# Kernel tuning notes

Hardware: AMD Instinct MI355X
Metric: run time of the kernel (lower is better)

## Reference

```python
import jax, jax.numpy as jnp
import numpy as np

N = 65536      # voxels
NFIX = 4096    # fixed-BC voxels (x == 0)
H = 128        # MLP hidden width
NFORCE = 4096  # force-surface points
E0 = 1.0
NU = 0.3
PENAL = 3.0
EM_V = 1e-3    # element volume
L_FIX = 0.05   # BC ramp length for analytical fixed-BC scale
K_FIX = E0 * 100.0
NUM_HUTCH = 50


def mlp(params, x):
    W1, b1, W2, b2, W3, b3, W4, b4 = params
    h = jnp.tanh(x @ W1 + b1)
    h = jnp.tanh(h @ W2 + b2)
    h = jnp.tanh(h @ W3 + b3)
    return h @ W4 + b4


def bc_scale(coord):
    # analytical fixed-BC scale: 0 exactly on the fixed face (x==0), ramps to 1
    return jnp.clip(coord[..., 0] / L_FIX, 0.0, 1.0)


def hutchinson_trace(params, coords, key, num_samples=NUM_HUTCH):
    # tr(J J^T) estimate via v^T J J^T v = ||J^T v||^2, batched VJPs (replaces
    # the per-sample autograd.grad python loop).
    out, vjp_fn = jax.vjp(lambda p: mlp(p, coords), params)

    def step(acc, k):
        v = jax.random.normal(k, out.shape, dtype=out.dtype)
        (g,) = vjp_fn(v)
        flat = jnp.concatenate([x.reshape(-1) for x in jax.tree_util.tree_leaves(g)])
        return acc + flat @ flat, None

    keys = jax.random.split(key, num_samples)
    tot, _ = jax.lax.scan(step, jnp.float32(0.0), keys)
    return tot / num_samples


def setup_inputs() -> dict:
    key = jax.random.key(0)
    ks = jax.random.split(key, 12)
    coord = jax.random.uniform(ks[0], (N, 3), dtype=jnp.float32)
    coord = coord.at[:, 0].set(0.02 + 0.98 * coord[:, 0])  # free voxels: x > 0
    coord = coord.at[:NFIX, 0].set(0.0)                    # fixed voxels: x == 0
    xPhys_m = jax.random.uniform(ks[1], (N, 1), dtype=jnp.float32)
    def lin(k, fi, fo):
        return jax.random.normal(k, (fi, fo), dtype=jnp.float32) / jnp.sqrt(jnp.float32(fi))
    W1 = lin(ks[2], 3, H); b1 = jnp.zeros((H,), jnp.float32)
    W2 = lin(ks[3], H, H); b2 = jnp.zeros((H,), jnp.float32)
    W3 = lin(ks[4], H, H); b3 = jnp.zeros((H,), jnp.float32)
    W4 = lin(ks[5], H, 3); b4 = jnp.zeros((3,), jnp.float32)
    force_coords = jax.random.uniform(ks[6], (NFORCE, 3), dtype=jnp.float32)
    F_vector = jax.random.normal(ks[7], (3,), dtype=jnp.float32)
    return dict(xPhys_m=xPhys_m, coord=coord, W1=W1, b1=b1, W2=W2, b2=b2,
                W3=W3, b3=b3, W4=W4, b4=b4, force_coords=force_coords,
                F_vector=F_vector, n_fix=NFIX)


def reference(xPhys_m, coord, W1, b1, W2, b2, W3, b3, W4, b4,
              force_coords, F_vector, n_fix):
    params = (W1, b1, W2, b2, W3, b3, W4, b4)

    u = mlp(params, coord)                       # [N,3] displacements
    scale = bc_scale(coord)                      # [N]
    fixed_mask = (scale == 0.0)

    # fixed-BC penalty energy
    u_fix = u * fixed_mask[:, None].astype(u.dtype)
    E_fix_all = xPhys_m ** PENAL * 0.5 * K_FIX * jnp.sum(u_fix ** 2, axis=1, keepdims=True)
    n_fix_ratio = jnp.float32(n_fix) / jnp.float32(N)
    E_fix = jnp.mean(E_fix_all[:n_fix]) * n_fix_ratio * EM_V

    # NTK-based adaptive weight via Hutchinson trace (detached, like .item())
    hkey = jax.random.key(42)
    ku, kr = jax.random.split(hkey)
    tr_uu = hutchinson_trace(params, coord[:n_fix], ku)
    tr_rr = hutchinson_trace(params, coord[n_fix:], kr)
    lam_fix = jax.lax.stop_gradient(jnp.clip(tr_rr / (tr_uu + 1e-12), 1e-3, 1e3))

    # per-voxel displacement Jacobian J[n, i, j] = d u_i / d coord_j  (batched
    # fwd-mode replaces three autograd.grad calls)
    J = jax.vmap(jax.jacfwd(lambda c: mlp(params, c)))(coord)  # [N,3,3]
    ux = J[:, 1, :]   # grads of u[:,1] (u0 in source)
    uy = J[:, 0, :]   # grads of u[:,0] (u1 in source)
    uz = J[:, 2, :]
    eps11 = ux[:, 1]
    eps12 = 0.5 * ux[:, 0] + 0.5 * uy[:, 1]
    eps13 = 0.5 * ux[:, 2] + 0.5 * uz[:, 1]
    eps22 = uy[:, 0]
    eps23 = 0.5 * uy[:, 2] + 0.5 * uz[:, 0]
    eps33 = uz[:, 2]

    lame_mu = E0 / (2.0 * (1.0 + NU))
    lame_lambda = E0 * NU / ((1.0 + NU) * (1.0 - 2.0 * NU))
    tr_strain = eps11 + eps22 + eps33
    sq_diag = eps11 * eps11 + eps22 * eps22 + eps33 * eps33
    energy = (0.5 * lame_lambda * tr_strain * tr_strain
              + lame_mu * (sq_diag + 2.0 * (eps12 * eps12 + eps13 * eps13 + eps23 * eps23)))
    energy = energy[:, None] * xPhys_m ** PENAL   # [N,1]
    energy_c = energy * 2.0
    energy_ans = EM_V * jnp.mean(energy)

    force_l = jnp.sum(mlp(params, force_coords) @ F_vector)

    loss = energy_ans - force_l + lam_fix * E_fix
    return (loss, energy_c, u)
```

## Files before the change

### kernel.cpp

```cpp
#include <hip/hip_runtime.h>
#include <math.h>

typedef __bf16 bf16x8 __attribute__((ext_vector_type(8)));
typedef __bf16 bf16x4 __attribute__((ext_vector_type(4)));
typedef float f32x4 __attribute__((ext_vector_type(4)));

#define HDIM 128
#define NTHREADS 512

#define EMV 0.001f
#define LFIX 0.05f
#define KFIX 100.0f
#define LAMBDA_L 0.5769230769230769f
#define MU_L 0.3846153846153846f

__device__ __forceinline__ int swb(int r, int blk) {
    return (r << 7) + ((blk ^ (r & 7)) << 3);
}
__device__ __forceinline__ int swb32(int r, int g) {
    return (r << 5) + ((g ^ ((r >> 1) & 3)) << 3);
}

__device__ __forceinline__ float fast_tanh(float x) {
    float e = __expf(2.f * x);
    return 1.f - 2.f * __builtin_amdgcn_rcpf(e + 1.f);
}

__device__ __forceinline__ float wred(float v) {
#pragma unroll
    for (int off = 32; off > 0; off >>= 1) v += __shfl_down(v, off, 64);
    return v;
}

template <int NB, int CT0, int CT1>
__device__ __forceinline__ void gemm_f8(const bf16x8 (&aw)[4],
                                        __bf16* const* inb, __bf16* const* outb,
                                        const float* __restrict__ bsL,
                                        int wid, int l15, int q) {
    f32x4 acc[NB][CT1 - CT0];
#pragma unroll
    for (int b = 0; b < NB; ++b)
#pragma unroll
        for (int c = 0; c < CT1 - CT0; ++c) acc[b][c] = (f32x4){0.f, 0.f, 0.f, 0.f};

#pragma unroll
    for (int s = 0; s < 4; ++s)
#pragma unroll
        for (int b = 0; b < NB; ++b)
#pragma unroll
            for (int c = CT0; c < CT1; ++c) {
                bf16x8 bfr = *(const bf16x8*)(inb[b] + swb(c * 16 + l15, s * 4 + q));
                acc[b][c - CT0] = __builtin_amdgcn_mfma_f32_16x16x32_bf16(
                    aw[s], bfr, acc[b][c - CT0], 0, 0, 0);
            }
    __syncthreads();
    const int n0 = wid * 16 + q * 4;
    float4 bv = *(const float4*)(bsL + n0);
    float bias4[4] = {bv.x, bv.y, bv.z, bv.w};
#pragma unroll
    for (int c = CT0; c < CT1; ++c) {
        const int p = c * 16 + l15;
        const int widx = swb(p, n0 >> 3) + (n0 & 7);
        bf16x4 hv;
        float fct[4];
#pragma unroll
        for (int i = 0; i < 4; ++i) {
            float h = fast_tanh(acc[0][c - CT0][i] + bias4[i]);
            hv[i] = (__bf16)h;
            fct[i] = 1.f - h * h;
        }
        *(bf16x4*)(outb[0] + widx) = hv;
#pragma unroll
        for (int b = 1; b < NB; ++b) {
            bf16x4 ov;
#pragma unroll
            for (int i = 0; i < 4; ++i) ov[i] = (__bf16)(acc[b][c - CT0][i] * fct[i]);
            *(bf16x4*)(outb[b] + widx) = ov;
        }
    }
}

template <int NB>
__device__ __forceinline__ void gemm_tr8(const float* __restrict__ Wg, __bf16* Wst,
                                         __bf16* const* bufs,
                                         const __bf16* __restrict__ href,
                                         int wid, int l15, int q, int tid) {
    f32x4 acc[NB][2];
#pragma unroll
    for (int b = 0; b < NB; ++b) {
        acc[b][0] = (f32x4){0.f, 0.f, 0.f, 0.f};
        acc[b][1] = (f32x4){0.f, 0.f, 0.f, 0.f};
    }
#pragma unroll
    for (int c = 0; c < 4; ++c) {
        __syncthreads();
        {
            int j = tid >> 2, k8 = tid & 3;
            const float4* src = (const float4*)(Wg + j * HDIM + c * 32 + k8 * 8);
            float4 v0 = src[0], v1 = src[1];
            bf16x8 pk = {(__bf16)v0.x, (__bf16)v0.y, (__bf16)v0.z, (__bf16)v0.w,
                         (__bf16)v1.x, (__bf16)v1.y, (__bf16)v1.z, (__bf16)v1.w};
            *(bf16x8*)(Wst + swb32(j, k8)) = pk;
        }
        __syncthreads();
        bf16x8 afr = *(const bf16x8*)(Wst + swb32(wid * 16 + l15, q));
#pragma unroll
        for (int b = 0; b < NB; ++b) {
            bf16x8 b0 = *(const bf16x8*)(bufs[b] + swb(l15, c * 4 + q));
            acc[b][0] = __builtin_amdgcn_mfma_f32_16x16x32_bf16(afr, b0, acc[b][0], 0, 0, 0);
            bf16x8 b1 = *(const bf16x8*)(bufs[b] + swb(16 + l15, c * 4 + q));
            acc[b][1] = __builtin_amdgcn_mfma_f32_16x16x32_bf16(afr, b1, acc[b][1], 0, 0, 0);
        }
    }
    __syncthreads();
    const int n0 = wid * 16 + q * 4;
#pragma unroll
    for (int ct = 0; ct < 2; ++ct) {
        const int p = ct * 16 + l15;
        const int widx = swb(p, n0 >> 3) + (n0 & 7);
        bf16x4 hv = *(const bf16x4*)(href + widx);
        float fct[4];
#pragma unroll
        for (int i = 0; i < 4; ++i) {
            float h = (float)hv[i];
            fct[i] = 1.f - h * h;
        }
#pragma unroll
        for (int b = 0; b < NB; ++b) {
            bf16x4 ov;
#pragma unroll
            for (int i = 0; i < 4; ++i) ov[i] = (__bf16)(acc[b][ct][i] * fct[i]);
            *(bf16x4*)(bufs[b] + widx) = ov;
        }
    }
}

__device__ __forceinline__ void dnorms8(const __bf16* a, const __bf16* b, const __bf16* c2,
                                        float* npart, int tid) {
    int p = tid & 31, cc = tid >> 5;
    bf16x8 v0 = *(const bf16x8*)(a + swb(p, cc));
    bf16x8 v1 = *(const bf16x8*)(b + swb(p, cc));
    bf16x8 v2 = *(const bf16x8*)(c2 + swb(p, cc));
    float s0 = 0.f, s1 = 0.f, s2 = 0.f;
#pragma unroll
    for (int e = 0; e < 8; ++e) {
        float f0 = (float)v0[e], f1 = (float)v1[e], f2 = (float)v2[e];
        s0 += f0 * f0;
        s1 += f1 * f1;
        s2 += f2 * f2;
    }
    npart[(0 + cc) * 32 + p] = s0;
    npart[(16 + cc) * 32 + p] = s1;
    npart[(32 + cc) * 32 + p] = s2;
}

__device__ __forceinline__ float sum16(const float* npart, int buf, int p) {
    float d = 0.f;
#pragma unroll
    for (int i = 0; i < 16; ++i) d += npart[(buf * 16 + i) * 32 + p];
    return d;
}
__device__ __forceinline__ float sum48(const float* npart, int p) {
    float d = 0.f;
#pragma unroll
    for (int i = 0; i < 48; ++i) d += npart[i * 32 + p];
    return d;
}

__global__ void __launch_bounds__(NTHREADS, 4) pinn_all(
    const float* __restrict__ xPhys, const float* __restrict__ coord,
    const float* __restrict__ W1, const float* __restrict__ b1,
    const float* __restrict__ W2, const float* __restrict__ b2,
    const float* __restrict__ W3, const float* __restrict__ b3,
    const float* __restrict__ W4, const float* __restrict__ b4,
    const float* __restrict__ fc, const float* __restrict__ Fv,
    const int* __restrict__ nfixp,
    float* __restrict__ energy_c_out, float* __restrict__ u_out,
    float* __restrict__ acc, int nm32, int nmain64, int ntrb, int NF) {
    __shared__ __align__(16) __bf16 pool[32768];
    __shared__ __align__(16) __bf16 W4p[16 * HDIM];
    __shared__ __align__(16) float W1s[4 * HDIM];
    __shared__ __align__(16) float W4ts[3 * HDIM];
    __shared__ __align__(16) float gls[64 * 12];
    __shared__ __align__(16) float uls[64 * 4];
    __shared__ float nh1s[32], nh2s[32], nh3s[32];

    const int tid = threadIdx.x;
    const int lane = tid & 63, wid = tid >> 6, l15 = lane & 15, q = lane >> 4;
    const int bi = blockIdx.x;
    const int nfixv = nfixp[0];

    int ttile = -1;
    if (bi < ntrb) {
        const int nfull = nfixv >> 5;
        const int cm = (nfixv & 31) ? 1 : 0;
        const int c1 = (nfull + 7) >> 3;
        int t;
        if (bi < c1) {
            t = bi << 3;
        } else if (cm && bi == c1) {
            t = nfull;
        } else {
            const int rr0 = nfull + cm;
            const int f0 = rr0 + ((8 - (rr0 & 15) + 16) & 15);
            t = f0 + ((bi - c1 - cm) << 4);
        }
        if (t >= nm32) return;
        ttile = t;
    }

    float px0, px1, px2;
    if (bi < ntrb) {
        const float* cp = coord + (ttile * 32 + (lane & 31)) * 3;
        px0 = cp[0]; px1 = cp[1]; px2 = cp[2];
    } else if (bi < ntrb + nmain64) {
        const float* cp = coord + ((bi - ntrb) * 64 + lane) * 3;
        px0 = cp[0]; px1 = cp[1]; px2 = cp[2];
    } else {
        int pp = (bi - ntrb - nmain64) * 64 + lane;
        if (pp >= NF) pp = NF - 1;
        const float* cp = fc + pp * 3;
        px0 = cp[0]; px1 = cp[1]; px2 = cp[2];
    }

    for (int i = tid; i < 3 * HDIM; i += NTHREADS) W1s[i] = W1[i];
    if (tid < HDIM) W1s[3 * HDIM + tid] = b1[tid];
    if (tid < 3 * HDIM) W4ts[tid] = W4[(tid & 127) * 3 + (tid >> 7)];
    if (tid < 256) {
        int o = tid >> 4, blk = tid & 15, j0 = blk * 8;
        bf16x8 pk;
#pragma unroll
        for (int e = 0; e < 8; ++e) pk[e] = (__bf16)((o < 3) ? W4[(j0 + e) * 3 + o] : 0.f);
        *(bf16x8*)(W4p + swb(o, blk)) = pk;
    }
    bf16x8 aw2[4], aw3[4];
#pragma unroll
    for (int s = 0; s < 4; ++s) {
        const int kb = s * 32 + q * 8;
        const int n = wid * 16 + l15;
        bf16x8 v2, v3;
#pragma unroll
        for (int e = 0; e < 8; ++e) {
            v2[e] = (__bf16)W2[(kb + e) * HDIM + n];
            v3[e] = (__bf16)W3[(kb + e) * HDIM + n];
        }
        aw2[s] = v2;
        aw3[s] = v3;
    }
    __syncthreads();

    if (bi < ntrb) {
        const int base = ttile * 32;
        __bf16* H1 = pool;
        __bf16* H2 = pool + 4096;
        __bf16* H3 = pool + 8192;
        __bf16* T0 = pool + 12288;
        __bf16* T1 = pool + 16384;
        __bf16* T2 = pool + 20480;
        __bf16* WST = pool + 24576;
        float* npart = (float*)(pool + 28672);

        {
            const int p = lane & 31, sub = lane >> 5;
            const int blk = wid * 2 + sub, j0 = blk * 8;
            bf16x8 hv, t0v, t1v, t2v;
#pragma unroll
            for (int jj = 0; jj < 8; ++jj) {
                int j = j0 + jj;
                float w0 = W1s[j], w1 = W1s[HDIM + j], w2 = W1s[2 * HDIM + j];
                float z = W1s[3 * HDIM + j] + px0 * w0 + px1 * w1 + px2 * w2;
                float h = fast_tanh(z);
                float fct = 1.f - h * h;
                hv[jj] = (__bf16)h;
                t0v[jj] = (__bf16)(fct * w0);
                t1v[jj] = (__bf16)(fct * w1);
                t2v[jj] = (__bf16)(fct * w2);
            }
            int wi = swb(p, blk);
            *(bf16x8*)(H1 + wi) = hv;
            *(bf16x8*)(T0 + wi) = t0v;
            *(bf16x8*)(T1 + wi) = t1v;
            *(bf16x8*)(T2 + wi) = t2v;
        }
        __syncthreads();
        {
            __bf16* ib[4] = {H1, T0, T1, T2};
            __bf16* ob[4] = {H2, T0, T1, T2};
            gemm_f8<4, 0, 2>(aw2, ib, ob, b2, wid, l15, q);
        }
        __syncthreads();
        {
            __bf16* ib[4] = {H2, T0, T1, T2};
            __bf16* ob[4] = {H3, T0, T1, T2};
            gemm_f8<4, 0, 2>(aw3, ib, ob, b3, wid, l15, q);
        }
        __syncthreads();

        dnorms8(H1, H2, H3, npart, tid);
        __syncthreads();
        if (tid < 32) {
            nh1s[tid] = sum16(npart, 0, tid);
            nh2s[tid] = sum16(npart, 1, tid);
            nh3s[tid] = sum16(npart, 2, tid);
        }
        __syncthreads();
        {
            const int p = lane & 31, sub = lane >> 5;
            const int blk = wid * 2 + sub, j0 = blk * 8;
            bf16x8 h3v = *(const bf16x8*)(H3 + swb(p, blk));
            bf16x8 d0, d1, d2;
#pragma unroll
            for (int e = 0; e < 8; ++e) {
                float h = (float)h3v[e];
                float fct = 1.f - h * h;
                d0[e] = (__bf16)(fct * W4ts[j0 + e]);
                d1[e] = (__bf16)(fct * W4ts[HDIM + j0 + e]);
                d2[e] = (__bf16)(fct * W4ts[2 * HDIM + j0 + e]);
            }
            int wi = swb(p, blk);
            *(bf16x8*)(T0 + wi) = d0;
            *(bf16x8*)(T1 + wi) = d1;
            *(bf16x8*)(T2 + wi) = d2;
        }
        __syncthreads();
        float s_acc = 0.f;
        dnorms8(T0, T1, T2, npart, tid);
        __syncthreads();
        if (tid < 32) s_acc = sum48(npart, tid) * (1.f + nh2s[tid]);
        {
            __bf16* ib[3] = {T0, T1, T2};
            gemm_tr8<3>(W3, WST, ib, H2, wid, l15, q, tid);
        }
        __syncthreads();
        dnorms8(T0, T1, T2, npart, tid);
        __syncthreads();
        if (tid < 32) s_acc += sum48(npart, tid) * (1.f + nh1s[tid]);
        {
            __bf16* ib[3] = {T0, T1, T2};
            gemm_tr8<3>(W2, WST, ib, H1, wid, l15, q, tid);
        }
        __syncthreads();
        dnorms8(T0, T1, T2, npart, tid);
        __syncthreads();
        if (tid < 64) {
            float su = 0.f, sr = 0.f, cu = 0.f, cr = 0.f;
            if (tid < 32) {
                int p = tid;
                float nx = px0 * px0 + px1 * px1 + px2 * px2;
                float s = s_acc + sum48(npart, p) * (1.f + nx) + 3.f * (nh3s[p] + 1.f);
                bool uu = (base + p) < nfixv;
                su = uu ? s : 0.f;
                sr = uu ? 0.f : s;
                cu = uu ? 1.f : 0.f;
                cr = uu ? 0.f : 1.f;
            }
            su = wred(su);
            sr = wred(sr);
            cu = wred(cu);
            cr = wred(cr);
            if (tid == 0) {
                atomicAdd(acc + 3, su);
                atomicAdd(acc + 4, sr);
                atomicAdd(acc + 5, cu);
                atomicAdd(acc + 6, cr);
            }
        }
    } else if (bi < ntrb + nmain64) {
        const int base = (bi - ntrb) * 64;
        __bf16* HF = pool;
        __bf16* TF0 = pool + 8192;
        __bf16* TF1 = pool + 16384;
        __bf16* TF2 = pool + 24576;

        {
            const int p = lane;
#pragma unroll
            for (int it2 = 0; it2 < 2; ++it2) {
                const int blk = it2 * 8 + wid, j0 = blk * 8;
                bf16x8 hv, t0v, t1v, t2v;
#pragma unroll
                for (int jj = 0; jj < 8; ++jj) {
                    int j = j0 + jj;
                    float w0 = W1s[j], w1 = W1s[HDIM + j], w2 = W1s[2 * HDIM + j];
                    float z = W1s[3 * HDIM + j] + px0 * w0 + px1 * w1 + px2 * w2;
                    float h = fast_tanh(z);
                    float fct = 1.f - h * h;
                    hv[jj] = (__bf16)h;
                    t0v[jj] = (__bf16)(fct * w0);
                    t1v[jj] = (__bf16)(fct * w1);
                    t2v[jj] = (__bf16)(fct * w2);
                }
                int wi = swb(p, blk);
                *(bf16x8*)(HF + wi) = hv;
                *(bf16x8*)(TF0 + wi) = t0v;
                *(bf16x8*)(TF1 + wi) = t1v;
                *(bf16x8*)(TF2 + wi) = t2v;
            }
        }
        __syncthreads();
        {
            __bf16* ib[4] = {HF, TF0, TF1, TF2};
            gemm_f8<4, 0, 2>(aw2, ib, ib, b2, wid, l15, q);
            gemm_f8<4, 2, 4>(aw2, ib, ib, b2, wid, l15, q);
        }
        __syncthreads();
        {
            __bf16* ib[4] = {HF, TF0, TF1, TF2};
            gemm_f8<4, 0, 2>(aw3, ib, ib, b3, wid, l15, q);
            gemm_f8<4, 2, 4>(aw3, ib, ib, b3, wid, l15, q);
        }
        __syncthreads();

        {
            f32x4 ha0 = (f32x4){0.f, 0.f, 0.f, 0.f};
            f32x4 ha1 = (f32x4){0.f, 0.f, 0.f, 0.f};
            if (wid < 4) {
                const int ct = wid;
#pragma unroll
                for (int s = 0; s < 4; ++s) {
                    int kb = s * 4 + q;
                    bf16x8 af = *(const bf16x8*)(W4p + swb(l15, kb));
                    bf16x8 bA = *(const bf16x8*)(HF + swb(ct * 16 + l15, kb));
                    ha0 = __builtin_amdgcn_mfma_f32_16x16x32_bf16(af, bA, ha0, 0, 0, 0);
                    bf16x8 bB = *(const bf16x8*)(TF0 + swb(ct * 16 + l15, kb));
                    ha1 = __builtin_amdgcn_mfma_f32_16x16x32_bf16(af, bB, ha1, 0, 0, 0);
                }
                if (q == 0) {
                    int p = ct * 16 + l15;
#pragma unroll
                    for (int o = 0; o < 3; ++o) {
                        float uv = ha0[o] + b4[o];
                        uls[p * 4 + o] = uv;
                        u_out[(base + p) * 3 + o] = uv;
                    }
#pragma unroll
                    for (int o = 0; o < 3; ++o) gls[p * 12 + o] = ha1[o];
                }
            } else {
                const int ct = wid - 4;
#pragma unroll
                for (int s = 0; s < 4; ++s) {
                    int kb = s * 4 + q;
                    bf16x8 af = *(const bf16x8*)(W4p + swb(l15, kb));
                    bf16x8 bA = *(const bf16x8*)(TF1 + swb(ct * 16 + l15, kb));
                    ha0 = __builtin_amdgcn_mfma_f32_16x16x32_bf16(af, bA, ha0, 0, 0, 0);
                    bf16x8 bB = *(const bf16x8*)(TF2 + swb(ct * 16 + l15, kb));
                    ha1 = __builtin_amdgcn_mfma_f32_16x16x32_bf16(af, bB, ha1, 0, 0, 0);
                }
                if (q == 0) {
                    int p = ct * 16 + l15;
#pragma unroll
                    for (int o = 0; o < 3; ++o) gls[p * 12 + 3 + o] = ha0[o];
#pragma unroll
                    for (int o = 0; o < 3; ++o) gls[p * 12 + 6 + o] = ha1[o];
                }
            }
        }
        __syncthreads();

        if (tid < 64) {
            int p = tid;
            float xp = xPhys[base + p];
            float xp3 = xp * xp * xp;
            float sc = fminf(fmaxf(px0 * (1.f / LFIX), 0.f), 1.f);
            float ef = 0.f;
            if ((base + p) < nfixv && sc == 0.f) {
                float u0 = uls[p * 4], u1 = uls[p * 4 + 1], u2 = uls[p * 4 + 2];
                ef = xp3 * 0.5f * KFIX * (u0 * u0 + u1 * u1 + u2 * u2);
            }
            float g00 = gls[p * 12 + 0], g01 = gls[p * 12 + 1], g02 = gls[p * 12 + 2];
            float g10 = gls[p * 12 + 3], g11 = gls[p * 12 + 4], g12 = gls[p * 12 + 5];
            float g20 = gls[p * 12 + 6], g21 = gls[p * 12 + 7], g22 = gls[p * 12 + 8];
            float e11 = g11, e22 = g00, e33 = g22;
            float e12 = 0.5f * (g01 + g10);
            float e13 = 0.5f * (g21 + g12);
            float e23 = 0.5f * (g20 + g02);
            float tr = e11 + e22 + e33;
            float en = 0.5f * LAMBDA_L * tr * tr +
                       MU_L * (e11 * e11 + e22 * e22 + e33 * e33 +
                               2.f * (e12 * e12 + e13 * e13 + e23 * e23));
            float exp3 = en * xp3;
            energy_c_out[base + p] = 2.f * exp3;
            float er = exp3;
            ef = wred(ef);
            er = wred(er);
            if (tid == 0) {
                atomicAdd(acc + 1, ef);
                atomicAdd(acc + 0, er);
            }
        }
    } else {
        const int fbase = (bi - ntrb - nmain64) * 64;
        __bf16* HF = pool;
        {
#pragma unroll
            for (int it2 = 0; it2 < 2; ++it2) {
                const int blk = it2 * 8 + wid, j0 = blk * 8;
                bf16x8 hv;
#pragma unroll
                for (int jj = 0; jj < 8; ++jj) {
                    int j = j0 + jj;
                    float z = W1s[3 * HDIM + j] + px0 * W1s[j] + px1 * W1s[HDIM + j] +
                              px2 * W1s[2 * HDIM + j];
                    hv[jj] = (__bf16)fast_tanh(z);
                }
                *(bf16x8*)(HF + swb(lane, blk)) = hv;
            }
        }
        __syncthreads();
        {
            __bf16* ib[1] = {HF};
            gemm_f8<1, 0, 2>(aw2, ib, ib, b2, wid, l15, q);
            gemm_f8<1, 2, 4>(aw2, ib, ib, b2, wid, l15, q);
        }
        __syncthreads();
        {
            __bf16* ib[1] = {HF};
            gemm_f8<1, 0, 2>(aw3, ib, ib, b3, wid, l15, q);
            gemm_f8<1, 2, 4>(aw3, ib, ib, b3, wid, l15, q);
        }
        __syncthreads();
        if (wid < 4) {
            const int ct = wid;
            f32x4 ha = (f32x4){0.f, 0.f, 0.f, 0.f};
#pragma unroll
            for (int s = 0; s < 4; ++s) {
                int kb = s * 4 + q;
                bf16x8 af = *(const bf16x8*)(W4p + swb(l15, kb));
                bf16x8 bf_ = *(const bf16x8*)(HF + swb(ct * 16 + l15, kb));
                ha = __builtin_amdgcn_mfma_f32_16x16x32_bf16(af, bf_, ha, 0, 0, 0);
            }
            if (q == 0) {
                int p = ct * 16 + l15;
#pragma unroll
                for (int o = 0; o < 3; ++o) uls[p * 4 + o] = ha[o] + b4[o];
            }
        }
        __syncthreads();
        if (tid < 64) {
            float fsum = 0.f;
            if (fbase + tid < NF)
                fsum = uls[tid * 4] * Fv[0] + uls[tid * 4 + 1] * Fv[1] +
                       uls[tid * 4 + 2] * Fv[2];
            fsum = wred(fsum);
            if (tid == 0) atomicAdd(acc + 2, fsum);
        }
    }
}

__global__ void pinn_final(const float* __restrict__ acc, float* __restrict__ out,
                           int Ntot, const int* __restrict__ nfixp) {
    float es = acc[0], ef = acc[1], fl = acc[2];
    float su = acc[3], sr = acc[4], cu = acc[5], cr = acc[6];
    float nfix = (float)nfixp[0];
    float tu = su / fmaxf(cu, 1.f) * nfix;
    float tr = sr / fmaxf(cr, 1.f) * ((float)Ntot - nfix);
    float energy_ans = EMV * (es / (float)Ntot);
    float E_fix = ef * EMV / (float)Ntot;
    float lam = tr / (tu + 1e-12f);
    lam = fminf(fmaxf(lam, 0.001f), 1000.f);
    out[0] = energy_ans - fl + lam * E_fix;
}

extern "C" void kernel_launch(void* const* d_in, const int* in_sizes, int n_in,
                              void* d_out, int out_size, void* d_ws, size_t ws_size,
                              hipStream_t stream) {
    const float* xPhys = (const float*)d_in[0];
    const float* coord = (const float*)d_in[1];
    const float* W1 = (const float*)d_in[2];
    const float* b1 = (const float*)d_in[3];
    const float* W2 = (const float*)d_in[4];
    const float* b2 = (const float*)d_in[5];
    const float* W3 = (const float*)d_in[6];
    const float* b3 = (const float*)d_in[7];
    const float* W4 = (const float*)d_in[8];
    const float* b4 = (const float*)d_in[9];
    const float* fc = (const float*)d_in[10];
    const float* Fv = (const float*)d_in[11];
    const int* nfix = (const int*)d_in[12];

    const int N = in_sizes[0];
    const int NF = in_sizes[10] / 3;
    float* out = (float*)d_out;
    float* acc = (float*)d_ws;

    const int nm32 = N / 32;
    const int nmain64 = N / 64;
    const int ntrb = nm32 / 8 + 2;
    const int nforce64 = (NF + 63) / 64;
    const int nblocks = ntrb + nmain64 + nforce64;
    (void)hipMemsetAsync(acc, 0, 8 * sizeof(float), stream);
    pinn_all<<<dim3(nblocks), dim3(NTHREADS), 0, stream>>>(
        xPhys, coord, W1, b1, W2, b2, W3, b3, W4, b4, fc, Fv, nfix,
        out + 1, out + 1 + N, acc, nm32, nmain64, ntrb, NF);
    pinn_final<<<dim3(1), dim3(1), 0, stream>>>(acc, out, N, nfix);
}
```

Measured before the change: 138.4 us.

## Retile main-path layer GEMMs into 32x32 per-wave blocks with per-buffer passes

Each wave now keeps W2/W3 fragments for two 16-column output tiles (a 32-wide column block) and computes a 2x2 tile block over 32 points, so every B fragment loaded from LDS feeds two MFMAs. The main 64-point path processes the hidden activations and the three tangent buffers in separate passes, keeping the tanh derivative factors in registers instead of one combined multi-buffer GEMM split into two halves. This is meant to cut LDS read traffic per MFMA. In exchange it adds more barriers (one per pass) and doubles the weight-fragment register footprint, which may lower occupancy; the other paths select one half of the fragments by wave parity.

```diff
diff --git a/kernel.cpp b/kernel.cpp
--- a/kernel.cpp
+++ b/kernel.cpp
@@ -32,8 +32,59 @@
     return v;
 }
 
+template <int PASS>
+__device__ __forceinline__ void fwpass(const bf16x8 (&aw)[4][2], __bf16* buf,
+                                       const float* __restrict__ bsL,
+                                       float (&fct)[2][2][4],
+                                       int cb, int rb, int l15, int q) {
+    f32x4 acc[2][2];
+#pragma unroll
+    for (int r = 0; r < 2; ++r)
+#pragma unroll
+        for (int ct = 0; ct < 2; ++ct) acc[r][ct] = (f32x4){0.f, 0.f, 0.f, 0.f};
+#pragma unroll
+    for (int s = 0; s < 4; ++s)
+#pragma unroll
+        for (int ct = 0; ct < 2; ++ct) {
+            bf16x8 bfr = *(const bf16x8*)(buf + swb(rb * 32 + ct * 16 + l15, s * 4 + q));
+#pragma unroll
+            for (int r = 0; r < 2; ++r)
+                acc[r][ct] = __builtin_amdgcn_mfma_f32_16x16x32_bf16(
+                    aw[s][r], bfr, acc[r][ct], 0, 0, 0);
+        }
+    __syncthreads();
+#pragma unroll
+    for (int r = 0; r < 2; ++r) {
+        const int n0 = cb * 32 + r * 16 + q * 4;
+        float bias4[4];
+        if (PASS == 0) {
+            float4 bv = *(const float4*)(bsL + n0);
+            bias4[0] = bv.x; bias4[1] = bv.y; bias4[2] = bv.z; bias4[3] = bv.w;
+        }
+#pragma unroll
+        for (int ct = 0; ct < 2; ++ct) {
+            const int p = rb * 32 + ct * 16 + l15;
+            const int widx = swb(p, n0 >> 3) + (n0 & 7);
+            bf16x4 ov;
+            if (PASS == 0) {
+#pragma unroll
+                for (int i = 0; i < 4; ++i) {
+                    float h = fast_tanh(acc[r][ct][i] + bias4[i]);
+                    ov[i] = (__bf16)h;
+                    fct[r][ct][i] = 1.f - h * h;
+                }
+            } else {
+#pragma unroll
+                for (int i = 0; i < 4; ++i)
+                    ov[i] = (__bf16)(acc[r][ct][i] * fct[r][ct][i]);
+            }
+            *(bf16x4*)(buf + widx) = ov;
+        }
+    }
+}
+
 template <int NB, int CT0, int CT1>
-__device__ __forceinline__ void gemm_f8(const bf16x8 (&aw)[4],
+__device__ __forceinline__ void gemm_f8(const bf16x8 (&aw)[4][2], int rsel,
                                         __bf16* const* inb, __bf16* const* outb,
                                         const float* __restrict__ bsL,
                                         int wid, int l15, int q) {
@@ -44,15 +95,17 @@
         for (int c = 0; c < CT1 - CT0; ++c) acc[b][c] = (f32x4){0.f, 0.f, 0.f, 0.f};
 
 #pragma unroll
-    for (int s = 0; s < 4; ++s)
+    for (int s = 0; s < 4; ++s) {
+        bf16x8 af = rsel ? aw[s][1] : aw[s][0];
 #pragma unroll
         for (int b = 0; b < NB; ++b)
 #pragma unroll
             for (int c = CT0; c < CT1; ++c) {
                 bf16x8 bfr = *(const bf16x8*)(inb[b] + swb(c * 16 + l15, s * 4 + q));
                 acc[b][c - CT0] = __builtin_amdgcn_mfma_f32_16x16x32_bf16(
-                    aw[s], bfr, acc[b][c - CT0], 0, 0, 0);
-            }
+                    af, bfr, acc[b][c - CT0], 0, 0, 0);
+            }
+    }
     __syncthreads();
     const int n0 = wid * 16 + q * 4;
     float4 bv = *(const float4*)(bsL + n0);
@@ -233,24 +286,27 @@
         for (int e = 0; e < 8; ++e) pk[e] = (__bf16)((o < 3) ? W4[(j0 + e) * 3 + o] : 0.f);
         *(bf16x8*)(W4p + swb(o, blk)) = pk;
     }
-    bf16x8 aw2[4], aw3[4];
-#pragma unroll
-    for (int s = 0; s < 4; ++s) {
-        const int kb = s * 32 + q * 8;
-        const int n = wid * 16 + l15;
-        bf16x8 v2, v3;
-#pragma unroll
-        for (int e = 0; e < 8; ++e) {
-            v2[e] = (__bf16)W2[(kb + e) * HDIM + n];
-            v3[e] = (__bf16)W3[(kb + e) * HDIM + n];
-        }
-        aw2[s] = v2;
-        aw3[s] = v3;
-    }
+    bf16x8 aw2[4][2], aw3[4][2];
+#pragma unroll
+    for (int s = 0; s < 4; ++s)
+#pragma unroll
+        for (int r = 0; r < 2; ++r) {
+            const int kb = s * 32 + q * 8;
+            const int n = (wid >> 1) * 32 + r * 16 + l15;
+            bf16x8 v2, v3;
+#pragma unroll
+            for (int e = 0; e < 8; ++e) {
+                v2[e] = (__bf16)W2[(kb + e) * HDIM + n];
+                v3[e] = (__bf16)W3[(kb + e) * HDIM + n];
+            }
+            aw2[s][r] = v2;
+            aw3[s][r] = v3;
+        }
     __syncthreads();
 
     if (bi < ntrb) {
         const int base = ttile * 32;
+        const int rsel = wid & 1;
         __bf16* H1 = pool;
         __bf16* H2 = pool + 4096;
         __bf16* H3 = pool + 8192;
@@ -286,13 +342,13 @@
         {
             __bf16* ib[4] = {H1, T0, T1, T2};
             __bf16* ob[4] = {H2, T0, T1, T2};
-            gemm_f8<4, 0, 2>(aw2, ib, ob, b2, wid, l15, q);
+            gemm_f8<4, 0, 2>(aw2, rsel, ib, ob, b2, wid, l15, q);
         }
         __syncthreads();
         {
             __bf16* ib[4] = {H2, T0, T1, T2};
             __bf16* ob[4] = {H3, T0, T1, T2};
-            gemm_f8<4, 0, 2>(aw3, ib, ob, b3, wid, l15, q);
+            gemm_f8<4, 0, 2>(aw3, rsel, ib, ob, b3, wid, l15, q);
         }
         __syncthreads();
 
@@ -367,6 +423,7 @@
         }
     } else if (bi < ntrb + nmain64) {
         const int base = (bi - ntrb) * 64;
+        const int cb = wid >> 1, rb = wid & 1;
         __bf16* HF = pool;
         __bf16* TF0 = pool + 8192;
         __bf16* TF1 = pool + 16384;
@@ -398,17 +455,15 @@
             }
         }
         __syncthreads();
-        {
-            __bf16* ib[4] = {HF, TF0, TF1, TF2};
-            gemm_f8<4, 0, 2>(aw2, ib, ib, b2, wid, l15, q);
-            gemm_f8<4, 2, 4>(aw2, ib, ib, b2, wid, l15, q);
-        }
-        __syncthreads();
-        {
-            __bf16* ib[4] = {HF, TF0, TF1, TF2};
-            gemm_f8<4, 0, 2>(aw3, ib, ib, b3, wid, l15, q);
-            gemm_f8<4, 2, 4>(aw3, ib, ib, b3, wid, l15, q);
-        }
+        float fct[2][2][4];
+        fwpass<0>(aw2, HF, b2, fct, cb, rb, l15, q);
+        fwpass<1>(aw2, TF0, b2, fct, cb, rb, l15, q);
+        fwpass<1>(aw2, TF1, b2, fct, cb, rb, l15, q);
+        fwpass<1>(aw2, TF2, b2, fct, cb, rb, l15, q);
+        fwpass<0>(aw3, HF, b3, fct, cb, rb, l15, q);
+        fwpass<1>(aw3, TF0, b3, fct, cb, rb, l15, q);
+        fwpass<1>(aw3, TF1, b3, fct, cb, rb, l15, q);
+        fwpass<1>(aw3, TF2, b3, fct, cb, rb, l15, q);
         __syncthreads();
 
         {
@@ -491,6 +546,7 @@
         }
     } else {
         const int fbase = (bi - ntrb - nmain64) * 64;
+        const int rsel = wid & 1;
         __bf16* HF = pool;
         {
 #pragma unroll
@@ -510,14 +566,14 @@
         __syncthreads();
         {
             __bf16* ib[1] = {HF};
-            gemm_f8<1, 0, 2>(aw2, ib, ib, b2, wid, l15, q);
-            gemm_f8<1, 2, 4>(aw2, ib, ib, b2, wid, l15, q);
+            gemm_f8<1, 0, 2>(aw2, rsel, ib, ib, b2, wid, l15, q);
+            gemm_f8<1, 2, 4>(aw2, rsel, ib, ib, b2, wid, l15, q);
         }
         __syncthreads();
         {
             __bf16* ib[1] = {HF};
-            gemm_f8<1, 0, 2>(aw3, ib, ib, b3, wid, l15, q);
-            gemm_f8<1, 2, 4>(aw3, ib, ib, b3, wid, l15, q);
+            gemm_f8<1, 0, 2>(aw3, rsel, ib, ib, b3, wid, l15, q);
+            gemm_f8<1, 2, 4>(aw3, rsel, ib, ib, b3, wid, l15, q);
         }
         __syncthreads();
         if (wid < 4) {
```

Measured after the change: 188.6 us. 36.3% more time.
